# Kernel optimization log

Hardware: AMD Instinct MI355X
Metric: run time of the kernel (lower is better)

The kernel has to match this reference:

```python
import jax, jax.numpy as jnp
import numpy as np

N_NODES = 100000
N_EDGES = 1600000
IN_DIM = 128
HID = 64
NUM_GRAPHS = 2048
NUM_CLASSES = 1


def setup_inputs() -> dict:
    key = jax.random.key(0)
    ks = jax.random.split(key, 16)
    x = jax.random.normal(ks[0], (N_NODES, IN_DIM), dtype=jnp.float32)
    edge_index = jax.random.randint(ks[1], (2, N_EDGES), 0, N_NODES, dtype=jnp.int64)
    batch_index = jnp.sort(jax.random.randint(ks[2], (N_NODES,), 0, NUM_GRAPHS, dtype=jnp.int64))
    # GCNConv weights (glorot-ish scale)
    def lin(k, fi, fo):
        return jax.random.normal(k, (fi, fo), dtype=jnp.float32) / np.sqrt(fi)
    W1 = lin(ks[3], IN_DIM, HID); b1 = jnp.zeros((HID,), jnp.float32)
    W2 = lin(ks[4], HID, HID);    b2 = jnp.zeros((HID,), jnp.float32)
    W3 = lin(ks[5], HID, HID);    b3 = jnp.zeros((HID,), jnp.float32)
    W4 = lin(ks[6], HID, HID);    b4 = jnp.zeros((HID,), jnp.float32)
    Wout = lin(ks[7], 2 * HID, NUM_CLASSES); bout = jnp.zeros((NUM_CLASSES,), jnp.float32)
    return {"x": x, "edge_index": edge_index, "batch_index": batch_index,
            "W1": W1, "b1": b1, "W2": W2, "b2": b2, "W3": W3, "b3": b3,
            "W4": W4, "b4": b4, "Wout": Wout, "bout": bout}


def _gcn_conv(x, W, b, src, dst, norm, n):
    # PyG GCNConv: linear transform, then D^-1/2 (A+I) D^-1/2 aggregation, then bias
    h = x @ W                                   # [N, F_out]
    msg = h[src] * norm[:, None]                # [E+N, F_out] gather + scale
    agg = jax.ops.segment_sum(msg, dst, num_segments=n)
    return agg + b


def reference(x, edge_index, batch_index, W1, b1, W2, b2, W3, b3, W4, b4, Wout, bout):
    n = x.shape[0]
    loops = jnp.arange(n, dtype=edge_index.dtype)
    src = jnp.concatenate([edge_index[0], loops])  # add self-loops
    dst = jnp.concatenate([edge_index[1], loops])
    deg = jax.ops.segment_sum(jnp.ones_like(dst, dtype=x.dtype), dst, num_segments=n)
    dis = jax.lax.rsqrt(deg)                       # deg >= 1 due to self-loops
    norm = dis[src] * dis[dst]

    h = x
    for (W, b) in ((W1, b1), (W2, b2), (W3, b3), (W4, b4)):
        h = jax.nn.relu(_gcn_conv(h, W, b, src, dst, norm, n))

    # global mean pool + global max pool per graph
    counts = jax.ops.segment_sum(jnp.ones((n,), h.dtype), batch_index, num_segments=NUM_GRAPHS)
    mean = jax.ops.segment_sum(h, batch_index, num_segments=NUM_GRAPHS) / jnp.maximum(counts, 1.0)[:, None]
    mx = jax.ops.segment_max(h, batch_index, num_segments=NUM_GRAPHS)
    mx = jnp.where(counts[:, None] > 0, mx, 0.0)
    pooled = jnp.concatenate([mean, mx], axis=1)   # [G, 2*HID]

    out = pooled @ Wout + bout                     # [G, 1]
    return (out, pooled)
```

## Files before the change

kernel.cpp:

```cpp
#include <hip/hip_runtime.h>
#include <hip/hip_fp16.h>

#define N_NODES 100000
#define IN_DIM 128
#define HID 64
#define NUM_GRAPHS 2048
#define CNE_MAX (1600000 + 7 * N_NODES)
#define BROWS 128
#define NBUCK ((N_NODES + BROWS - 1) / BROWS)
#define NCHUNK 256
#define TOTP (NBUCK * NCHUNK)
#define CAP 4096

typedef _Float16 h8 __attribute__((ext_vector_type(8)));
typedef float f4 __attribute__((ext_vector_type(4)));

__device__ __forceinline__ float2 u2f2(unsigned u) {
    __half2 h = *reinterpret_cast<__half2*>(&u);
    return __half22float2(h);
}


__global__ __launch_bounds__(256) void hist_partial(const int* __restrict__ dst,
                                                    int* __restrict__ partial,
                                                    int E, int chunk,
                                                    unsigned* __restrict__ padA,
                                                    unsigned* __restrict__ padB) {
    __shared__ int lh[NBUCK];
    int t = threadIdx.x, c = blockIdx.x;
    if (c == 0) {
        if (t < 32) padA[t] = 0;
        else if (t < 64) padB[t - 32] = 0;
    }
    for (int b = t; b < NBUCK; b += 256) lh[b] = 0;
    __syncthreads();
    int lo = c * chunk, hi = min(lo + chunk, E);
    for (int i = lo + t; i < hi; i += 256) atomicAdd(&lh[dst[i] >> 7], 1);
    __syncthreads();
    for (int b = t; b < NBUCK; b += 256) partial[b * NCHUNK + c] = lh[b];
}

__global__ void scan1(const int* __restrict__ counts, int* __restrict__ out1,
                      int* __restrict__ bsum, int n, int pad8) {
    __shared__ int s[256];
    int t = threadIdx.x;
    int base = blockIdx.x * 1024 + t * 4;
    int v[4];
#pragma unroll
    for (int i = 0; i < 4; i++) {
        int c = (base + i < n) ? counts[base + i] : 0;
        v[i] = pad8 ? ((c + 7) & ~7) : c;
    }
    int tsum = v[0] + v[1] + v[2] + v[3];
    s[t] = tsum;
    __syncthreads();
    for (int off = 1; off < 256; off <<= 1) {
        int tv = (t >= off) ? s[t - off] : 0;
        __syncthreads();
        s[t] += tv;
        __syncthreads();
    }
    int excl = s[t] - tsum;
    if (t == 255) bsum[blockIdx.x] = s[255];
    int run = excl;
#pragma unroll
    for (int i = 0; i < 4; i++) {
        run += v[i];
        if (base + i < n) out1[base + i] = run;
    }
}

__device__ __forceinline__ int inline_bscan(const int* __restrict__ bsum, int nb, int* s) {
    int t = threadIdx.x;
    int v = (t < nb) ? bsum[t] : 0;
    s[t] = v;
    __syncthreads();
    for (int off = 1; off < 256; off <<= 1) {
        int tv = (t >= off) ? s[t - off] : 0;
        __syncthreads();
        s[t] += tv;
        __syncthreads();
    }
    int excl = s[t] - v;
    __syncthreads();
    s[t] = excl;
    __syncthreads();
    return excl;
}

__global__ __launch_bounds__(256) void scan3(int* __restrict__ row_ptr,
                                             const int* __restrict__ bsum, int nb, int n) {
    __shared__ int s[256];
    inline_bscan(bsum, nb, s);
    int i = blockIdx.x * blockDim.x + threadIdx.x;
    if (i == 0) row_ptr[0] = 0;
    if (i < n) row_ptr[i + 1] += s[i >> 10];
}

__global__ __launch_bounds__(256) void scan3p(const int* __restrict__ partial,
                                              const int* __restrict__ pincl,
                                              const int* __restrict__ bsum, int nb,
                                              int* __restrict__ base,
                                              int* __restrict__ part_off, int E) {
    __shared__ int s[256];
    inline_bscan(bsum, nb, s);
    int i = blockIdx.x * blockDim.x + threadIdx.x;
    if (i < TOTP) {
        int v = pincl[i] + s[i >> 10] - partial[i];
        base[i] = v;
        if ((i & (NCHUNK - 1)) == 0) part_off[i / NCHUNK] = v;
    }
    if (i == 0) part_off[NBUCK] = E;
}

__global__ __launch_bounds__(256) void partition_edges(const int* __restrict__ src,
                                                       const int* __restrict__ dst,
                                                       const int* __restrict__ base,
                                                       unsigned* __restrict__ part,
                                                       int E, int chunk) {
    __shared__ int cur[NBUCK];
    int t = threadIdx.x, c = blockIdx.x;
    for (int b = t; b < NBUCK; b += 256) cur[b] = base[b * NCHUNK + c];
    __syncthreads();
    int lo = c * chunk, hi = min(lo + chunk, E);
    for (int i = lo + t; i < hi; i += 256) {
        int s = src[i], d = dst[i];
        int pos = atomicAdd(&cur[d >> 7], 1);
        part[pos] = (unsigned)s | ((unsigned)(d & (BROWS - 1)) << 17);
    }
}

__global__ __launch_bounds__(256) void deg_dis(const unsigned* __restrict__ part,
                                               const int* __restrict__ part_off,
                                               int* __restrict__ pdeg,
                                               float* __restrict__ dis, int n) {
    __shared__ int cnt[BROWS];
    int t = threadIdx.x, b = blockIdx.x;
    int r0 = b * BROWS;
    if (t < BROWS) cnt[t] = 0;
    __syncthreads();
    for (int i = part_off[b] + t; i < part_off[b + 1]; i += 256)
        atomicAdd(&cnt[part[i] >> 17], 1);
    __syncthreads();
    int nrows = min(BROWS, n - r0);
    if (t < nrows) {
        int dg = cnt[t];
        pdeg[r0 + t] = dg;
        dis[r0 + t] = rsqrtf((float)(dg + 1));
    }
}

__global__ __launch_bounds__(256) void build_csr(const unsigned* __restrict__ part,
                                                 const int* __restrict__ part_off,
                                                 const int* __restrict__ row_ptr,
                                                 unsigned* __restrict__ cne, int n) {
    __shared__ int fill[BROWS];
    __shared__ unsigned stage[CAP];
    int b = blockIdx.x;
    int r0 = b * BROWS;
    int t = threadIdx.x;
    int nrows = min(BROWS, n - r0);
    int base = row_ptr[r0];
    int region = row_ptr[r0 + nrows] - base;
    for (int r = t; r < nrows; r += 256) fill[r] = row_ptr[r0 + r] - base;
    int i0 = part_off[b], i1 = part_off[b + 1];
    if (region <= CAP) {
        for (int i = t; i < region; i += 256) stage[i] = (unsigned)N_NODES << 7;
        __syncthreads();
        for (int i = i0 + t; i < i1; i += 256) {
            unsigned pe = part[i];
            int pos = atomicAdd(&fill[pe >> 17], 1);
            stage[pos] = (pe & 0x1FFFFu) << 7;
        }
        __syncthreads();
        for (int i = t; i < region; i += 256) cne[base + i] = stage[i];
    } else {
        for (int i = t; i < region; i += 256) cne[base + i] = (unsigned)N_NODES << 7;
        __syncthreads();
        for (int i = i0 + t; i < i1; i += 256) {
            unsigned pe = part[i];
            int pos = atomicAdd(&fill[pe >> 17], 1);
            cne[base + pos] = (pe & 0x1FFFFu) << 7;
        }
    }
}


template <int K, typename XT>
__global__ __launch_bounds__(256) void gemm_mfma(const XT* __restrict__ X,
                                                 const float* __restrict__ W,
                                                 const float* __restrict__ dis,
                                                 __half* __restrict__ out, int n) {
    const int KS = K / 32;
    int wave = threadIdx.x >> 6, lane = threadIdx.x & 63;
    int quad = lane >> 4, l16 = lane & 15;
    h8 b[4][KS];
#pragma unroll
    for (int ct = 0; ct < 4; ct++)
#pragma unroll
        for (int ks = 0; ks < KS; ks++)
#pragma unroll
            for (int j = 0; j < 8; j++)
                b[ct][ks][j] = (_Float16)W[(ks * 32 + quad * 8 + j) * HID + ct * 16 + l16];
    int ntile = n >> 4;
    int wpb = blockDim.x >> 6;
    int stride = gridDim.x * wpb;
    for (int rt = blockIdx.x * wpb + wave; rt < ntile; rt += stride) {
        int row0 = rt << 4;
        const XT* xr = X + (size_t)(row0 + l16) * K + quad * 8;
        f4 acc[4];
#pragma unroll
        for (int ct = 0; ct < 4; ct++) acc[ct] = (f4)(0.f);
#pragma unroll
        for (int ks = 0; ks < KS; ks++) {
            h8 a;
            if constexpr (__is_same(XT, float)) {
                float4 xa = *(const float4*)(xr + ks * 32);
                float4 xb = *(const float4*)(xr + ks * 32 + 4);
                a[0] = (_Float16)xa.x; a[1] = (_Float16)xa.y;
                a[2] = (_Float16)xa.z; a[3] = (_Float16)xa.w;
                a[4] = (_Float16)xb.x; a[5] = (_Float16)xb.y;
                a[6] = (_Float16)xb.z; a[7] = (_Float16)xb.w;
            } else {
                a = *(const h8*)(xr + ks * 32);
            }
#pragma unroll
            for (int ct = 0; ct < 4; ct++)
                acc[ct] = __builtin_amdgcn_mfma_f32_16x16x32_f16(a, b[ct][ks], acc[ct], 0, 0, 0);
        }
        int r0 = row0 + quad * 4;
        float4 dv = *(const float4*)(dis + r0);
        float dd[4] = {dv.x, dv.y, dv.z, dv.w};
#pragma unroll
        for (int reg = 0; reg < 4; reg++) {
            __half* orow = out + (size_t)(r0 + reg) * HID + l16;
            orow[0]  = __float2half(dd[reg] * acc[0][reg]);
            orow[16] = __float2half(dd[reg] * acc[1][reg]);
            orow[32] = __float2half(dd[reg] * acc[2][reg]);
            orow[48] = __float2half(dd[reg] * acc[3][reg]);
        }
    }
}

template <typename OutT>
__global__ __launch_bounds__(256) void aggregate4(const __half* __restrict__ tmp,
                                                  const float* __restrict__ dis,
                                                  const int* __restrict__ row_ptr,
                                                  const unsigned* __restrict__ cne,
                                                  const float* __restrict__ bias,
                                                  OutT* __restrict__ out, int n) {
    int wave = threadIdx.x >> 6, lane = threadIdx.x & 63;
    int m4 = lane & 15, rq = lane >> 4;
    const char* tb = (const char*)tmp + 8 * m4;
    float4 blv = *(const float4*)(bias + 4 * m4);
    int wpb = blockDim.x >> 6;
    int stride = gridDim.x * wpb;
    int ntask = n >> 2;
    const unsigned Z = (unsigned)N_NODES << 7;
    int t = blockIdx.x * wpb + wave;
    if (t >= ntask) return;
    int row = 4 * t + rq;
    int sE = row_ptr[row], eE = row_ptr[row + 1];
    uint4 A0, A1;
    if (sE < eE) {
        const uint4* ip0 = (const uint4*)(cne + sE);
        A0 = ip0[0]; A1 = ip0[1];
    } else {
        A0 = make_uint4(Z, Z, Z, Z); A1 = make_uint4(Z, Z, Z, Z);
    }
    while (true) {
        row = 4 * t + rq;
        float dr = dis[row];
        uint2 g0 = *(const uint2*)(tb + A0.x);
        uint2 g1 = *(const uint2*)(tb + A0.y);
        uint2 g2 = *(const uint2*)(tb + A0.z);
        uint2 g3 = *(const uint2*)(tb + A0.w);
        uint2 g4 = *(const uint2*)(tb + A1.x);
        uint2 g5 = *(const uint2*)(tb + A1.y);
        uint2 g6 = *(const uint2*)(tb + A1.z);
        uint2 g7 = *(const uint2*)(tb + A1.w);
        int tn = t + stride;
        int sN = 0, eN = 0;
        if (tn < ntask) {
            int rn = 4 * tn + rq;
            sN = row_ptr[rn]; eN = row_ptr[rn + 1];
        }
        int ng = (eE - sE) >> 3;
        float a0 = 0.f, a1 = 0.f, a2 = 0.f, a3 = 0.f;
        const uint4* ip = (const uint4*)(cne + sE);
        uint4 B0, B1;
        if (ng > 1) { B0 = ip[2]; B1 = ip[3]; }
        for (int g = 1; g < ng; g++) {
            uint2 u0 = *(const uint2*)(tb + B0.x);
            uint2 u1 = *(const uint2*)(tb + B0.y);
            uint2 u2 = *(const uint2*)(tb + B0.z);
            uint2 u3 = *(const uint2*)(tb + B0.w);
            uint2 u4 = *(const uint2*)(tb + B1.x);
            uint2 u5 = *(const uint2*)(tb + B1.y);
            uint2 u6 = *(const uint2*)(tb + B1.z);
            uint2 u7 = *(const uint2*)(tb + B1.w);
            if (g + 1 < ng) { B0 = ip[2 * g + 2]; B1 = ip[2 * g + 3]; }
            float2 f;
            f = u2f2(g0.x); a0 += f.x; a1 += f.y; f = u2f2(g0.y); a2 += f.x; a3 += f.y;
            f = u2f2(g1.x); a0 += f.x; a1 += f.y; f = u2f2(g1.y); a2 += f.x; a3 += f.y;
            f = u2f2(g2.x); a0 += f.x; a1 += f.y; f = u2f2(g2.y); a2 += f.x; a3 += f.y;
            f = u2f2(g3.x); a0 += f.x; a1 += f.y; f = u2f2(g3.y); a2 += f.x; a3 += f.y;
            f = u2f2(g4.x); a0 += f.x; a1 += f.y; f = u2f2(g4.y); a2 += f.x; a3 += f.y;
            f = u2f2(g5.x); a0 += f.x; a1 += f.y; f = u2f2(g5.y); a2 += f.x; a3 += f.y;
            f = u2f2(g6.x); a0 += f.x; a1 += f.y; f = u2f2(g6.y); a2 += f.x; a3 += f.y;
            f = u2f2(g7.x); a0 += f.x; a1 += f.y; f = u2f2(g7.y); a2 += f.x; a3 += f.y;
            g0 = u0; g1 = u1; g2 = u2; g3 = u3;
            g4 = u4; g5 = u5; g6 = u6; g7 = u7;
        }
        {
            float2 f;
            f = u2f2(g0.x); a0 += f.x; a1 += f.y; f = u2f2(g0.y); a2 += f.x; a3 += f.y;
            f = u2f2(g1.x); a0 += f.x; a1 += f.y; f = u2f2(g1.y); a2 += f.x; a3 += f.y;
            f = u2f2(g2.x); a0 += f.x; a1 += f.y; f = u2f2(g2.y); a2 += f.x; a3 += f.y;
            f = u2f2(g3.x); a0 += f.x; a1 += f.y; f = u2f2(g3.y); a2 += f.x; a3 += f.y;
            f = u2f2(g4.x); a0 += f.x; a1 += f.y; f = u2f2(g4.y); a2 += f.x; a3 += f.y;
            f = u2f2(g5.x); a0 += f.x; a1 += f.y; f = u2f2(g5.y); a2 += f.x; a3 += f.y;
            f = u2f2(g6.x); a0 += f.x; a1 += f.y; f = u2f2(g6.y); a2 += f.x; a3 += f.y;
            f = u2f2(g7.x); a0 += f.x; a1 += f.y; f = u2f2(g7.y); a2 += f.x; a3 += f.y;
        }
        if (sN < eN) {
            const uint4* ipn = (const uint4*)(cne + sN);
            A0 = ipn[0]; A1 = ipn[1];
        } else {
            A0 = make_uint4(Z, Z, Z, Z); A1 = make_uint4(Z, Z, Z, Z);
        }
        uint2 sv = *(const uint2*)(tb + (size_t)row * 128);
        float2 s01 = u2f2(sv.x), s23 = u2f2(sv.y);
        float v0 = fmaxf(dr * (s01.x + a0) + blv.x, 0.f);
        float v1 = fmaxf(dr * (s01.y + a1) + blv.y, 0.f);
        float v2 = fmaxf(dr * (s23.x + a2) + blv.z, 0.f);
        float v3 = fmaxf(dr * (s23.y + a3) + blv.w, 0.f);
        if constexpr (__is_same(OutT, __half)) {
            __half2 p01 = __floats2half2_rn(v0, v1);
            __half2 p23 = __floats2half2_rn(v2, v3);
            *(uint2*)((char*)out + (size_t)row * 128 + 8 * m4) =
                make_uint2(*(unsigned*)&p01, *(unsigned*)&p23);
        } else {
            *(float4*)(out + (size_t)row * HID + 4 * m4) = make_float4(v0, v1, v2, v3);
        }
        if (tn >= ntask) break;
        t = tn; sE = sN; eE = eN;
    }
}

__global__ __launch_bounds__(256) void pool_kernel(const float* __restrict__ h,
                                                   const int* __restrict__ batch,
                                                   const float* __restrict__ Wout,
                                                   const float* __restrict__ bout,
                                                   float* __restrict__ d_out, int n) {
    __shared__ float ssum[4][64];
    __shared__ float smax[4][64];
    int g = blockIdx.x;
    int wave = threadIdx.x >> 6, j = threadIdx.x & 63;
    int lo = 0, hi = n;
    while (lo < hi) { int mid = (lo + hi) >> 1; if (batch[mid] < g) lo = mid + 1; else hi = mid; }
    int start = lo;
    hi = n;
    while (lo < hi) { int mid = (lo + hi) >> 1; if (batch[mid] < g + 1) lo = mid + 1; else hi = mid; }
    int end = lo;

    float sum = 0.f, mx = 0.f;
    for (int i = start + wave; i < end; i += 4) {
        float v = h[(size_t)i * HID + j];
        sum += v;
        mx = fmaxf(mx, v);
    }
    ssum[wave][j] = sum;
    smax[wave][j] = mx;
    __syncthreads();
    if (wave == 0) {
        sum = (ssum[0][j] + ssum[1][j]) + (ssum[2][j] + ssum[3][j]);
        mx = fmaxf(fmaxf(smax[0][j], smax[1][j]), fmaxf(smax[2][j], smax[3][j]));
        float cnt = (float)(end - start);
        float mean = sum / fmaxf(cnt, 1.f);
        float* pooled = d_out + NUM_GRAPHS;
        pooled[(size_t)g * (2 * HID) + j] = mean;
        pooled[(size_t)g * (2 * HID) + HID + j] = mx;
        float c = mean * Wout[j] + mx * Wout[HID + j];
#pragma unroll
        for (int off = 32; off; off >>= 1) c += __shfl_down(c, off);
        if (j == 0) d_out[g] = c + bout[0];
    }
}


extern "C" void kernel_launch(void* const* d_in, const int* in_sizes, int n_in,
                              void* d_out, int out_size, void* d_ws, size_t ws_size,
                              hipStream_t stream) {
    const float* x    = (const float*)d_in[0];
    const int*   edge = (const int*)d_in[1];
    const int*   batch= (const int*)d_in[2];
    const float* W1 = (const float*)d_in[3];  const float* b1 = (const float*)d_in[4];
    const float* W2 = (const float*)d_in[5];  const float* b2 = (const float*)d_in[6];
    const float* W3 = (const float*)d_in[7];  const float* b3 = (const float*)d_in[8];
    const float* W4 = (const float*)d_in[9];  const float* b4 = (const float*)d_in[10];
    const float* Wout = (const float*)d_in[11]; const float* bout = (const float*)d_in[12];
    float* out = (float*)d_out;

    const int N = N_NODES;
    const int E = in_sizes[1] / 2;
    const int* src = edge;
    const int* dst = edge + E;
    const int chunk = (E + NCHUNK - 1) / NCHUNK;

    char* p = (char*)d_ws;
    auto alloc = [&](size_t bytes) -> char* {
        char* r = p;
        p += (bytes + 255) & ~(size_t)255;
        return r;
    };
    int*      pdeg     = (int*)alloc((size_t)N * 4);
    int*      row_ptr  = (int*)alloc((size_t)(N + 1) * 4);
    int*      partial  = (int*)alloc((size_t)TOTP * 4);
    int*      pincl    = (int*)alloc((size_t)TOTP * 4);
    int*      pbase    = (int*)alloc((size_t)TOTP * 4);
    int*      part_off = (int*)alloc((size_t)(NBUCK + 1) * 4);
    unsigned* part     = (unsigned*)alloc((size_t)1600000 * 4);
    unsigned* cne      = (unsigned*)alloc((size_t)CNE_MAX * 4);
    float*    dis      = (float*)alloc((size_t)N * 4);
    int*      bsum     = (int*)alloc(256 * 4);
    __half*   tmp      = (__half*)alloc((size_t)(N + 1) * HID * 2);
    float*    hA       = (float*)alloc((size_t)N * HID * 4);
    __half*   hH       = (__half*)hA;

    unsigned* padrow = (unsigned*)(tmp + (size_t)N * HID);
    hist_partial<<<NCHUNK, 256, 0, stream>>>(dst, partial, E, chunk, padrow, padrow);
    int nbp = (TOTP + 1023) / 1024;
    scan1<<<nbp, 256, 0, stream>>>(partial, pincl, bsum, TOTP, 0);
    scan3p<<<(TOTP + 255) / 256, 256, 0, stream>>>(partial, pincl, bsum, nbp, pbase, part_off, E);
    partition_edges<<<NCHUNK, 256, 0, stream>>>(src, dst, pbase, part, E, chunk);
    deg_dis<<<NBUCK, 256, 0, stream>>>(part, part_off, pdeg, dis, N);

    int nb = (N + 1023) / 1024;
    scan1<<<nb, 256, 0, stream>>>(pdeg, row_ptr + 1, bsum, N, 1);
    scan3<<<(N + 255) / 256, 256, 0, stream>>>(row_ptr, bsum, nb, N);
    build_csr<<<NBUCK, 256, 0, stream>>>(part, part_off, row_ptr, cne, N);

    const int AGG_BLOCKS = 2048;
    const int GEMM_BLOCKS = 1024;

    gemm_mfma<IN_DIM, float><<<GEMM_BLOCKS, 256, 0, stream>>>(x, W1, dis, tmp, N);
    aggregate4<__half><<<AGG_BLOCKS, 256, 0, stream>>>(tmp, dis, row_ptr, cne, b1, hH, N);
    gemm_mfma<HID, _Float16><<<GEMM_BLOCKS, 256, 0, stream>>>((_Float16*)hH, W2, dis, tmp, N);
    aggregate4<__half><<<AGG_BLOCKS, 256, 0, stream>>>(tmp, dis, row_ptr, cne, b2, hH, N);
    gemm_mfma<HID, _Float16><<<GEMM_BLOCKS, 256, 0, stream>>>((_Float16*)hH, W3, dis, tmp, N);
    aggregate4<__half><<<AGG_BLOCKS, 256, 0, stream>>>(tmp, dis, row_ptr, cne, b3, hH, N);
    gemm_mfma<HID, _Float16><<<GEMM_BLOCKS, 256, 0, stream>>>((_Float16*)hH, W4, dis, tmp, N);
    aggregate4<float><<<AGG_BLOCKS, 256, 0, stream>>>(tmp, dis, row_ptr, cne, b4, hA, N);

    pool_kernel<<<NUM_GRAPHS, 256, 0, stream>>>(hA, batch, Wout, bout, out, N);
}
```

Measured before the change: 346.3 us.

## Replace bucketed two-pass CSR build with global-atomic degree count and fill

The bucketed partition pipeline (histogram, partial scans, partition, per-bucket degree and LDS-staged CSR fill) is replaced by a global atomic per-node degree count, one row-pointer scan fused with dis and cursor computation, and an atomic scatter fill with separate zero-padding of each row's tail. This cuts the preprocessing from eight launches to a memset plus four kernels and removes the intermediate partition buffer. In exchange it relies on many contended global atomics and uncoalesced scattered writes, and the order of neighbours within each row now varies from run to run.

```diff
diff --git a/kernel.cpp b/kernel.cpp
--- a/kernel.cpp
+++ b/kernel.cpp
@@ -6,11 +6,6 @@
 #define HID 64
 #define NUM_GRAPHS 2048
 #define CNE_MAX (1600000 + 7 * N_NODES)
-#define BROWS 128
-#define NBUCK ((N_NODES + BROWS - 1) / BROWS)
-#define NCHUNK 256
-#define TOTP (NBUCK * NCHUNK)
-#define CAP 4096
 
 typedef _Float16 h8 __attribute__((ext_vector_type(8)));
 typedef float f4 __attribute__((ext_vector_type(4)));
@@ -21,23 +16,13 @@
 }
 
 
-__global__ __launch_bounds__(256) void hist_partial(const int* __restrict__ dst,
-                                                    int* __restrict__ partial,
-                                                    int E, int chunk,
-                                                    unsigned* __restrict__ padA,
-                                                    unsigned* __restrict__ padB) {
-    __shared__ int lh[NBUCK];
-    int t = threadIdx.x, c = blockIdx.x;
-    if (c == 0) {
-        if (t < 32) padA[t] = 0;
-        else if (t < 64) padB[t - 32] = 0;
-    }
-    for (int b = t; b < NBUCK; b += 256) lh[b] = 0;
-    __syncthreads();
-    int lo = c * chunk, hi = min(lo + chunk, E);
-    for (int i = lo + t; i < hi; i += 256) atomicAdd(&lh[dst[i] >> 7], 1);
-    __syncthreads();
-    for (int b = t; b < NBUCK; b += 256) partial[b * NCHUNK + c] = lh[b];
+__global__ __launch_bounds__(256) void deg_atomic(const int* __restrict__ dst,
+                                                  int* __restrict__ pdeg,
+                                                  unsigned* __restrict__ padrow, int E) {
+    int i = blockIdx.x * blockDim.x + threadIdx.x;
+    if (blockIdx.x == 0 && threadIdx.x < 32) padrow[threadIdx.x] = 0;
+    int stride = gridDim.x * blockDim.x;
+    for (int e = i; e < E; e += stride) atomicAdd(&pdeg[dst[e]], 1);
 }
 
 __global__ void scan1(const int* __restrict__ counts, int* __restrict__ out1,
@@ -70,7 +55,7 @@
     }
 }
 
-__device__ __forceinline__ int inline_bscan(const int* __restrict__ bsum, int nb, int* s) {
+__device__ __forceinline__ void inline_bscan(const int* __restrict__ bsum, int nb, int* s) {
     int t = threadIdx.x;
     int v = (t < nb) ? bsum[t] : 0;
     s[t] = v;
@@ -85,103 +70,44 @@
     __syncthreads();
     s[t] = excl;
     __syncthreads();
-    return excl;
-}
-
-__global__ __launch_bounds__(256) void scan3(int* __restrict__ row_ptr,
-                                             const int* __restrict__ bsum, int nb, int n) {
+}
+
+__global__ __launch_bounds__(256) void scan3d(int* __restrict__ row_ptr,
+                                              const int* __restrict__ bsum, int nb,
+                                              const int* __restrict__ pdeg,
+                                              int* __restrict__ cur,
+                                              float* __restrict__ dis, int n) {
     __shared__ int s[256];
     inline_bscan(bsum, nb, s);
     int i = blockIdx.x * blockDim.x + threadIdx.x;
     if (i == 0) row_ptr[0] = 0;
-    if (i < n) row_ptr[i + 1] += s[i >> 10];
-}
-
-__global__ __launch_bounds__(256) void scan3p(const int* __restrict__ partial,
-                                              const int* __restrict__ pincl,
-                                              const int* __restrict__ bsum, int nb,
-                                              int* __restrict__ base,
-                                              int* __restrict__ part_off, int E) {
-    __shared__ int s[256];
-    inline_bscan(bsum, nb, s);
+    if (i < n) {
+        int v = row_ptr[i + 1] + s[i >> 10];
+        row_ptr[i + 1] = v;
+        int dg = pdeg[i];
+        cur[i] = v - ((dg + 7) & ~7);
+        dis[i] = rsqrtf((float)(dg + 1));
+    }
+}
+
+__global__ __launch_bounds__(256) void fill_atomic(const int* __restrict__ src,
+                                                   const int* __restrict__ dst,
+                                                   int* __restrict__ cur,
+                                                   const int* __restrict__ row_ptr,
+                                                   const int* __restrict__ pdeg,
+                                                   unsigned* __restrict__ cne, int E, int n) {
     int i = blockIdx.x * blockDim.x + threadIdx.x;
-    if (i < TOTP) {
-        int v = pincl[i] + s[i >> 10] - partial[i];
-        base[i] = v;
-        if ((i & (NCHUNK - 1)) == 0) part_off[i / NCHUNK] = v;
-    }
-    if (i == 0) part_off[NBUCK] = E;
-}
-
-__global__ __launch_bounds__(256) void partition_edges(const int* __restrict__ src,
-                                                       const int* __restrict__ dst,
-                                                       const int* __restrict__ base,
-                                                       unsigned* __restrict__ part,
-                                                       int E, int chunk) {
-    __shared__ int cur[NBUCK];
-    int t = threadIdx.x, c = blockIdx.x;
-    for (int b = t; b < NBUCK; b += 256) cur[b] = base[b * NCHUNK + c];
-    __syncthreads();
-    int lo = c * chunk, hi = min(lo + chunk, E);
-    for (int i = lo + t; i < hi; i += 256) {
-        int s = src[i], d = dst[i];
-        int pos = atomicAdd(&cur[d >> 7], 1);
-        part[pos] = (unsigned)s | ((unsigned)(d & (BROWS - 1)) << 17);
-    }
-}
-
-__global__ __launch_bounds__(256) void deg_dis(const unsigned* __restrict__ part,
-                                               const int* __restrict__ part_off,
-                                               int* __restrict__ pdeg,
-                                               float* __restrict__ dis, int n) {
-    __shared__ int cnt[BROWS];
-    int t = threadIdx.x, b = blockIdx.x;
-    int r0 = b * BROWS;
-    if (t < BROWS) cnt[t] = 0;
-    __syncthreads();
-    for (int i = part_off[b] + t; i < part_off[b + 1]; i += 256)
-        atomicAdd(&cnt[part[i] >> 17], 1);
-    __syncthreads();
-    int nrows = min(BROWS, n - r0);
-    if (t < nrows) {
-        int dg = cnt[t];
-        pdeg[r0 + t] = dg;
-        dis[r0 + t] = rsqrtf((float)(dg + 1));
-    }
-}
-
-__global__ __launch_bounds__(256) void build_csr(const unsigned* __restrict__ part,
-                                                 const int* __restrict__ part_off,
-                                                 const int* __restrict__ row_ptr,
-                                                 unsigned* __restrict__ cne, int n) {
-    __shared__ int fill[BROWS];
-    __shared__ unsigned stage[CAP];
-    int b = blockIdx.x;
-    int r0 = b * BROWS;
-    int t = threadIdx.x;
-    int nrows = min(BROWS, n - r0);
-    int base = row_ptr[r0];
-    int region = row_ptr[r0 + nrows] - base;
-    for (int r = t; r < nrows; r += 256) fill[r] = row_ptr[r0 + r] - base;
-    int i0 = part_off[b], i1 = part_off[b + 1];
-    if (region <= CAP) {
-        for (int i = t; i < region; i += 256) stage[i] = (unsigned)N_NODES << 7;
-        __syncthreads();
-        for (int i = i0 + t; i < i1; i += 256) {
-            unsigned pe = part[i];
-            int pos = atomicAdd(&fill[pe >> 17], 1);
-            stage[pos] = (pe & 0x1FFFFu) << 7;
-        }
-        __syncthreads();
-        for (int i = t; i < region; i += 256) cne[base + i] = stage[i];
-    } else {
-        for (int i = t; i < region; i += 256) cne[base + i] = (unsigned)N_NODES << 7;
-        __syncthreads();
-        for (int i = i0 + t; i < i1; i += 256) {
-            unsigned pe = part[i];
-            int pos = atomicAdd(&fill[pe >> 17], 1);
-            cne[base + pos] = (pe & 0x1FFFFu) << 7;
-        }
+    int stride = gridDim.x * blockDim.x;
+    const unsigned Z = (unsigned)N_NODES << 7;
+    for (int e = i; e < E; e += stride) {
+        int d = dst[e];
+        int pos = atomicAdd(&cur[d], 1);
+        cne[pos] = (unsigned)src[e] << 7;
+    }
+    for (int r = i; r < n; r += stride) {
+        int dg = pdeg[r];
+        int end = row_ptr[r + 1];
+        for (int k = end - ((dg + 7) & ~7) + dg; k < end; k++) cne[k] = Z;
     }
 }
 
@@ -406,7 +332,6 @@
     const int E = in_sizes[1] / 2;
     const int* src = edge;
     const int* dst = edge + E;
-    const int chunk = (E + NCHUNK - 1) / NCHUNK;
 
     char* p = (char*)d_ws;
     auto alloc = [&](size_t bytes) -> char* {
@@ -416,11 +341,7 @@
     };
     int*      pdeg     = (int*)alloc((size_t)N * 4);
     int*      row_ptr  = (int*)alloc((size_t)(N + 1) * 4);
-    int*      partial  = (int*)alloc((size_t)TOTP * 4);
-    int*      pincl    = (int*)alloc((size_t)TOTP * 4);
-    int*      pbase    = (int*)alloc((size_t)TOTP * 4);
-    int*      part_off = (int*)alloc((size_t)(NBUCK + 1) * 4);
-    unsigned* part     = (unsigned*)alloc((size_t)1600000 * 4);
+    int*      cur      = (int*)alloc((size_t)N * 4);
     unsigned* cne      = (unsigned*)alloc((size_t)CNE_MAX * 4);
     float*    dis      = (float*)alloc((size_t)N * 4);
     int*      bsum     = (int*)alloc(256 * 4);
@@ -429,17 +350,13 @@
     __half*   hH       = (__half*)hA;
 
     unsigned* padrow = (unsigned*)(tmp + (size_t)N * HID);
-    hist_partial<<<NCHUNK, 256, 0, stream>>>(dst, partial, E, chunk, padrow, padrow);
-    int nbp = (TOTP + 1023) / 1024;
-    scan1<<<nbp, 256, 0, stream>>>(partial, pincl, bsum, TOTP, 0);
-    scan3p<<<(TOTP + 255) / 256, 256, 0, stream>>>(partial, pincl, bsum, nbp, pbase, part_off, E);
-    partition_edges<<<NCHUNK, 256, 0, stream>>>(src, dst, pbase, part, E, chunk);
-    deg_dis<<<NBUCK, 256, 0, stream>>>(part, part_off, pdeg, dis, N);
-
+
+    hipMemsetAsync(pdeg, 0, (size_t)N * 4, stream);
+    deg_atomic<<<2048, 256, 0, stream>>>(dst, pdeg, padrow, E);
     int nb = (N + 1023) / 1024;
     scan1<<<nb, 256, 0, stream>>>(pdeg, row_ptr + 1, bsum, N, 1);
-    scan3<<<(N + 255) / 256, 256, 0, stream>>>(row_ptr, bsum, nb, N);
-    build_csr<<<NBUCK, 256, 0, stream>>>(part, part_off, row_ptr, cne, N);
+    scan3d<<<(N + 255) / 256, 256, 0, stream>>>(row_ptr, bsum, nb, pdeg, cur, dis, N);
+    fill_atomic<<<2048, 256, 0, stream>>>(src, dst, cur, row_ptr, pdeg, cne, E, N);
 
     const int AGG_BLOCKS = 2048;
     const int GEMM_BLOCKS = 1024;
```

New measurement: 504.5 us. 45.7% more time.
